# Optimization experiments

Hardware: AMD Instinct MI355X
Metric: run time of the kernel (lower is better)

Reference implementation:

```python
import jax, jax.numpy as jnp
import numpy as np

N_USERS = 100_000
N_ITEMS = 200_000
N_EDGES = 1_000_000
D = 64        # in_size == every layer_size
L = 3         # number of NGCF layers
B = 4096      # BPR batch
SLOPE = 0.2   # LeakyReLU negative slope
EPS = 1e-12   # F.normalize eps


def setup_inputs() -> dict:
    key = jax.random.key(0)
    ks = jax.random.split(key, 11)
    s = 1.0 / np.sqrt(D)  # xavier-ish scale
    return dict(
        user_feat=jax.random.normal(ks[0], (N_USERS, D), jnp.float32) * s,
        item_feat=jax.random.normal(ks[1], (N_ITEMS, D), jnp.float32) * s,
        W1=jax.random.normal(ks[2], (L, D, D), jnp.float32) * s,
        b1=jnp.zeros((L, D), jnp.float32),
        W2=jax.random.normal(ks[3], (L, D, D), jnp.float32) * s,
        b2=jnp.zeros((L, D), jnp.float32),
        edge_src=jax.random.randint(ks[4], (N_EDGES,), 0, N_USERS),
        edge_dst=jax.random.randint(ks[5], (N_EDGES,), 0, N_ITEMS),
        users=jax.random.randint(ks[6], (B,), 0, N_USERS),
        pos_items=jax.random.randint(ks[7], (B,), 0, N_ITEMS),
        neg_items=jax.random.randint(ks[8], (B,), 0, N_ITEMS),
    )


def _act_norm(h):
    # LeakyReLU(0.2) -> (dropout=identity, eval) -> row-wise L2 normalize
    h = jax.nn.leaky_relu(h, SLOPE)
    n = jnp.linalg.norm(h, axis=1, keepdims=True)
    return h / jnp.maximum(n, EPS)


def _ngcf_forward(user_feat, item_feat, W1, b1, W2, b2, edge_src, edge_dst):
    ones = jnp.ones((edge_src.shape[0],), user_feat.dtype)
    deg_u = jax.ops.segment_sum(ones, edge_src, num_segments=N_USERS)  # out-degree of users
    deg_i = jax.ops.segment_sum(ones, edge_dst, num_segments=N_ITEMS)  # in-degree of items
    norm = (deg_u[edge_src] * deg_i[edge_dst]) ** -0.5  # [E], same for both directions
    norm = norm[:, None]

    hu, hi = user_feat, item_feat
    u_embeds, i_embeds = [hu], [hi]
    for l in range(L):
        # per-edge elementwise product term (shared between both directions)
        p = hu[edge_src] * hi[edge_dst]            # [E, D]
        pw = p @ W2[l] + b2[l]                     # [E, D]
        # user -> item messages, summed per item
        m_i = norm * ((hu @ W1[l] + b1[l])[edge_src] + pw)
        # item -> user messages, summed per user
        m_u = norm * ((hi @ W1[l] + b1[l])[edge_dst] + pw)
        hi_new = jax.ops.segment_sum(m_i, edge_dst, num_segments=N_ITEMS)
        hu_new = jax.ops.segment_sum(m_u, edge_src, num_segments=N_USERS)
        hu, hi = _act_norm(hu_new), _act_norm(hi_new)
        u_embeds.append(hu)
        i_embeds.append(hi)

    user_embd = jnp.concatenate(u_embeds, axis=1)  # [N_USERS, D*(L+1)]
    item_embd = jnp.concatenate(i_embeds, axis=1)  # [N_ITEMS, D*(L+1)]
    return user_embd, item_embd


def reference(user_feat, item_feat, W1, b1, W2, b2,
              edge_src, edge_dst, users, pos_items, neg_items):
    user_embd, item_embd = _ngcf_forward(
        user_feat, item_feat, W1, b1, W2, b2, edge_src, edge_dst)
    return (user_embd[users], item_embd[pos_items], item_embd[neg_items])
```

## Files before the change

### kernel.cpp

```cpp
#include <hip/hip_runtime.h>

#define NU 100000
#define NI 200000
#define NE 1000000
#define NB 4096
#define CAP 16384
#define NBS 98
#define NBD 98
#define NTI (NI / 16)
#define NTU (NU / 16)

typedef __attribute__((ext_vector_type(8))) short bf16x8;
typedef __attribute__((ext_vector_type(4))) float f32x4;
typedef __attribute__((ext_vector_type(8))) unsigned short u16x8;

static __device__ __forceinline__ short f2bf(float f) {
  unsigned u = __builtin_bit_cast(unsigned, f);
  unsigned r = (u + 0x7fffu + ((u >> 16) & 1u)) >> 16;
  return (short)r;
}
static __device__ __forceinline__ float bf2f(unsigned short u) {
  return __builtin_bit_cast(float, ((unsigned)u) << 16);
}

__global__ __launch_bounds__(256) void binA_kernel(const int* __restrict__ src,
                                                   const int* __restrict__ dst,
                                                   int* __restrict__ gcur_s,
                                                   int* __restrict__ gcur_d,
                                                   int2* __restrict__ temp_s,
                                                   int2* __restrict__ temp_d) {
  __shared__ int lh[128], lbase[128], lpos[128];
  const int dir = blockIdx.x >> 9;
  const int cb = blockIdx.x & 511;
  const int lo = (int)(((long long)NE * cb) >> 9);
  const int hi = (int)(((long long)NE * (cb + 1)) >> 9);
  const int* key = dir ? dst : src;
  const int* oth = dir ? src : dst;
  int* gcur = dir ? gcur_d : gcur_s;
  int2* temp = dir ? temp_d : temp_s;
  const int shift = dir ? 11 : 10;
  const int tid = threadIdx.x;
  if (tid < 128) lh[tid] = 0;
  __syncthreads();
  for (int e = lo + tid; e < hi; e += 256) atomicAdd(&lh[key[e] >> shift], 1);
  __syncthreads();
  if (tid < 128) {
    const int c = lh[tid];
    lbase[tid] = c ? atomicAdd(&gcur[tid], c) : 0;
    lpos[tid] = 0;
  }
  __syncthreads();
  for (int e = lo + tid; e < hi; e += 256) {
    const int k = key[e];
    const int b = k >> shift;
    const int p = lbase[b] + atomicAdd(&lpos[b], 1);
    temp[(size_t)b * CAP + p] = make_int2(k, oth[e]);
  }
}

__global__ void bktscan_kernel(const int* __restrict__ gcur_s, const int* __restrict__ gcur_d,
                               int* __restrict__ bktofs_s, int* __restrict__ bktofs_d,
                               int* __restrict__ ofs_u, int* __restrict__ ofs_i) {
  const int t = threadIdx.x;
  if (t == 0) {
    int a = 0;
    for (int i = 0; i < NBS; ++i) { bktofs_s[i] = a; a += gcur_s[i]; }
    bktofs_s[NBS] = a;
    ofs_u[NU] = NE;
  }
  if (t == 1) {
    int a = 0;
    for (int i = 0; i < NBD; ++i) { bktofs_d[i] = a; a += gcur_d[i]; }
    bktofs_d[NBD] = a;
    ofs_i[NI] = NE;
  }
}

__global__ __launch_bounds__(256) void placeB_kernel(const int2* __restrict__ temp_s,
                                                     const int2* __restrict__ temp_d,
                                                     const int* __restrict__ gcur_s,
                                                     const int* __restrict__ gcur_d,
                                                     const int* __restrict__ bktofs_s,
                                                     const int* __restrict__ bktofs_d,
                                                     int* __restrict__ ofs_u, int* __restrict__ ofs_i,
                                                     float* __restrict__ rs_u, float* __restrict__ rs_i,
                                                     float* __restrict__ srs_u, float* __restrict__ srs_i,
                                                     int* __restrict__ by_src, int* __restrict__ by_dst) {
  __shared__ int cnt[2048];
  __shared__ int exc[2048];
  __shared__ int wsum[256];
  const bool isdst = blockIdx.x >= NBS;
  const int b = isdst ? (int)blockIdx.x - NBS : (int)blockIdx.x;
  const int shift = isdst ? 11 : 10;
  const int nodelo = b << shift;
  const int n = isdst ? NI : NU;
  const int2* temp = (isdst ? temp_d : temp_s) + (size_t)b * CAP;
  const int ecnt = (isdst ? gcur_d : gcur_s)[b];
  const int bbase = (isdst ? bktofs_d : bktofs_s)[b];
  int* ofs = isdst ? ofs_i : ofs_u;
  float* rs = isdst ? rs_i : rs_u;
  float* srs = isdst ? srs_i : srs_u;
  int* by = isdst ? by_dst : by_src;
  const int tid = threadIdx.x;
  const int NN = 1 << shift;

  for (int j = tid; j < NN; j += 256) cnt[j] = 0;
  __syncthreads();
  for (int k = tid; k < ecnt; k += 256) atomicAdd(&cnt[temp[k].x - nodelo], 1);
  __syncthreads();
  const int per = NN >> 8;
  int s = 0;
  for (int j = 0; j < per; ++j) s += cnt[tid * per + j];
  wsum[tid] = s;
  __syncthreads();
  for (int off = 1; off < 256; off <<= 1) {
    int t2 = (tid >= off) ? wsum[tid - off] : 0;
    __syncthreads();
    wsum[tid] += t2;
    __syncthreads();
  }
  int run = wsum[tid] - s;
  for (int j = 0; j < per; ++j) {
    const int idx = tid * per + j;
    exc[idx] = run;
    run += cnt[idx];
  }
  __syncthreads();
  for (int j = tid; j < NN; j += 256) {
    const int node = nodelo + j;
    if (node < n) {
      ofs[node] = bbase + exc[j];
      const int d = cnt[j];
      rs[node] = d > 0 ? rsqrtf((float)d) : 0.f;
      srs[node] = d > 0 ? sqrtf((float)d) : 0.f;
    }
  }
  __syncthreads();
  for (int j = tid; j < NN; j += 256) cnt[j] = exc[j];
  __syncthreads();
  for (int k = tid; k < ecnt; k += 256) {
    const int2 t2 = temp[k];
    const int p = bbase + atomicAdd(&cnt[t2.x - nodelo], 1);
    by[p] = t2.y;
  }
}

__global__ __launch_bounds__(256) void c_kernel(const int* __restrict__ ofs_i,
                                                const int* __restrict__ ofs_u,
                                                const int* __restrict__ by_dst,
                                                const int* __restrict__ by_src,
                                                const float* __restrict__ rs_u,
                                                const float* __restrict__ rs_i,
                                                float* __restrict__ c_i,
                                                float* __restrict__ c_u) {
  int r = blockIdx.x * 256 + threadIdx.x;
  if (r < NI) {
    const int lo = ofs_i[r], hi = ofs_i[r + 1];
    float s = 0.f;
    for (int k = lo; k < hi; ++k) s += rs_u[by_dst[k]];
    c_i[r] = rs_i[r] * s;
  } else if (r < NI + NU) {
    r -= NI;
    const int lo = ofs_u[r], hi = ofs_u[r + 1];
    float s = 0.f;
    for (int k = lo; k < hi; ++k) s += rs_i[by_src[k]];
    c_u[r] = rs_u[r] * s;
  }
}

__global__ __launch_bounds__(256) void conv_kernel(const float* __restrict__ uf,
                                                   const float* __restrict__ itf,
                                                   const float* __restrict__ rs_u,
                                                   const float* __restrict__ rs_i,
                                                   unsigned short* __restrict__ hsu,
                                                   unsigned short* __restrict__ hsi) {
  int i = blockIdx.x * 256 + threadIdx.x;
  const int n4u = NU * 16;
  const float* in;
  const float* rs;
  unsigned short* outp;
  int j;
  if (i < n4u) {
    in = uf; rs = rs_u; outp = hsu; j = i;
  } else if (i < n4u + NI * 16) {
    in = itf; rs = rs_i; outp = hsi; j = i - n4u;
  } else return;
  const float rsn = rs[j >> 4];
  float4 v = *(const float4*)&in[(size_t)j * 4];
  ushort4 o;
  o.x = (unsigned short)f2bf(v.x * rsn);
  o.y = (unsigned short)f2bf(v.y * rsn);
  o.z = (unsigned short)f2bf(v.z * rsn);
  o.w = (unsigned short)f2bf(v.w * rsn);
  *(ushort4*)&outp[(size_t)j * 4] = o;
}

__global__ __launch_bounds__(256) void layer_fused_kernel(const int* __restrict__ ofs_i,
                                                          const int* __restrict__ ofs_u,
                                                          const int* __restrict__ by_dst,
                                                          const int* __restrict__ by_src,
                                                          const float* __restrict__ rs_u,
                                                          const float* __restrict__ rs_i,
                                                          const float* __restrict__ c_i,
                                                          const float* __restrict__ c_u,
                                                          const unsigned short* __restrict__ hsu,
                                                          const unsigned short* __restrict__ hsi,
                                                          const float* __restrict__ W1,
                                                          const float* __restrict__ b1,
                                                          const float* __restrict__ W2,
                                                          const float* __restrict__ b2,
                                                          unsigned short* __restrict__ hsi_new,
                                                          unsigned short* __restrict__ hsu_new) {
  __shared__ unsigned short wlds[8192];
  const int tid = threadIdx.x;
  const int lane = tid & 63;
  const int row16 = lane & 15;
  const int kg = lane >> 4;
  for (int ch = tid; ch < 1024; ch += 256) {
    const int w = ch >> 9;
    const int rem = ch & 511;
    const int nb = rem >> 7, kb = (rem >> 6) & 1, l2 = rem & 63;
    const int r16 = l2 & 15, kg2 = l2 >> 4;
    const float* W = w ? W2 : W1;
    unsigned short* dstp = &wlds[ch * 8];
#pragma unroll
    for (int j = 0; j < 8; ++j)
      dstp[j] = (unsigned short)f2bf(W[(kb * 32 + kg2 * 8 + j) * 64 + nb * 16 + r16]);
  }
  __syncthreads();

  float bsum[4];
#pragma unroll
  for (int nb = 0; nb < 4; ++nb) bsum[nb] = b1[nb * 16 + row16] + b2[nb * 16 + row16];

  const int wid = (blockIdx.x * 256 + tid) >> 6;
  const int nwaves = (gridDim.x * 256) >> 6;

  for (int t = wid; t < NTI + NTU; t += nwaves) {
    const bool item = t < NTI;
    const int tt = item ? t : t - NTI;
    const int* ofs = item ? ofs_i : ofs_u;
    const int* pay = item ? by_dst : by_src;
    const float* rsw = item ? rs_i : rs_u;
    const float* cc = item ? c_i : c_u;
    const unsigned short* hs = item ? hsu : hsi;
    const unsigned short* hsown = item ? hsi : hsu;
    unsigned short* hsnew = item ? hsi_new : hsu_new;
    const int r0 = tt * 16;
    const int node = r0 + row16;

    const int lo = ofs[node], hiE = ofs[node + 1];
    int rounds = (hiE - lo + 3) >> 2;
#pragma unroll
    for (int m = 1; m < 16; m <<= 1) rounds = max(rounds, __shfl_xor(rounds, m));

    float a0[8] = {0.f, 0.f, 0.f, 0.f, 0.f, 0.f, 0.f, 0.f};
    float a1[8] = {0.f, 0.f, 0.f, 0.f, 0.f, 0.f, 0.f, 0.f};
    for (int rd = 0; rd < rounds; ++rd) {
      const int i0 = lo + rd * 4;
      int nb4[4];
      float wt[4];
#pragma unroll
      for (int s = 0; s < 4; ++s) {
        const int idx = i0 + s;
        nb4[s] = pay[min(idx, NE - 1)];
        wt[s] = (idx < hiE) ? 1.f : 0.f;
      }
      u16x8 h0[4], h1[4];
#pragma unroll
      for (int s = 0; s < 4; ++s) {
        const unsigned short* hp = hs + (size_t)nb4[s] * 64 + kg * 8;
        h0[s] = *(const u16x8*)hp;
        h1[s] = *(const u16x8*)(hp + 32);
      }
#pragma unroll
      for (int s = 0; s < 4; ++s)
#pragma unroll
        for (int j = 0; j < 8; ++j) {
          a0[j] += wt[s] * bf2f(h0[s][j]);
          a1[j] += wt[s] * bf2f(h1[s][j]);
        }
    }

    const float rsn = rsw[node];
    const float cnode = cc[node];
    const unsigned short* hp = hsown + (size_t)node * 64 + kg * 8;
    const u16x8 hv0 = *(const u16x8*)hp;
    const u16x8 hv1 = *(const u16x8*)(hp + 32);
    bf16x8 ag[2], ap[2];
#pragma unroll
    for (int j = 0; j < 8; ++j) {
      ag[0][j] = f2bf(a0[j] * rsn);
      ag[1][j] = f2bf(a1[j] * rsn);
      ap[0][j] = f2bf(a0[j] * bf2f(hv0[j]));
      ap[1][j] = f2bf(a1[j] * bf2f(hv1[j]));
    }

    f32x4 acc[4];
#pragma unroll
    for (int nb = 0; nb < 4; ++nb) acc[nb] = (f32x4){0.f, 0.f, 0.f, 0.f};
    const unsigned short* wl = wlds + lane * 8;
#pragma unroll
    for (int nb = 0; nb < 4; ++nb)
#pragma unroll
      for (int kb = 0; kb < 2; ++kb) {
        const bf16x8 w1f = *(const bf16x8*)(wl + ((0 * 4 + nb) * 2 + kb) * 512);
        const bf16x8 w2f = *(const bf16x8*)(wl + ((1 * 4 + nb) * 2 + kb) * 512);
        acc[nb] = __builtin_amdgcn_mfma_f32_16x16x32_bf16(ag[kb], w1f, acc[nb], 0, 0, 0);
        acc[nb] = __builtin_amdgcn_mfma_f32_16x16x32_bf16(ap[kb], w2f, acc[nb], 0, 0, 0);
      }

    float cv[4], rsrow[4];
#pragma unroll
    for (int reg = 0; reg < 4; ++reg) {
      cv[reg] = __shfl(cnode, kg * 4 + reg);
      rsrow[reg] = __shfl(rsn, kg * 4 + reg);
    }
    float v[4][4];
    float ss[4] = {0.f, 0.f, 0.f, 0.f};
#pragma unroll
    for (int nb = 0; nb < 4; ++nb)
#pragma unroll
      for (int reg = 0; reg < 4; ++reg) {
        float x = acc[nb][reg] + cv[reg] * bsum[nb];
        x = (x > 0.f) ? x : 0.2f * x;
        v[nb][reg] = x;
        ss[reg] += x * x;
      }
#pragma unroll
    for (int m = 1; m < 16; m <<= 1)
#pragma unroll
      for (int reg = 0; reg < 4; ++reg) ss[reg] += __shfl_xor(ss[reg], m);
#pragma unroll
    for (int reg = 0; reg < 4; ++reg) {
      const float invs = rsrow[reg] / fmaxf(sqrtf(ss[reg]), 1e-12f);
      const size_t rowbase = (size_t)(r0 + kg * 4 + reg) * 64;
#pragma unroll
      for (int nb = 0; nb < 4; ++nb)
        hsnew[rowbase + nb * 16 + row16] = (unsigned short)f2bf(v[nb][reg] * invs);
    }
  }
}

__global__ __launch_bounds__(256) void gather_f32_kernel(const float* __restrict__ hu,
                                                         const float* __restrict__ hi,
                                                         const int* __restrict__ users,
                                                         const int* __restrict__ pos,
                                                         const int* __restrict__ neg,
                                                         float* __restrict__ out) {
  int t = blockIdx.x * 256 + threadIdx.x;
  if (t >= 3 * NB * 64) return;
  int j = t & 63;
  int b = (t >> 6) & (NB - 1);
  int which = t / (NB * 64);
  int row = (which == 0) ? users[b] : ((which == 1) ? pos[b] : neg[b]);
  const float* h = (which == 0) ? hu : hi;
  out[(size_t)which * NB * 256 + (size_t)b * 256 + j] = h[(size_t)row * 64 + j];
}

__global__ __launch_bounds__(256) void gather_bf_kernel(const unsigned short* __restrict__ hsu,
                                                        const unsigned short* __restrict__ hsi,
                                                        const float* __restrict__ srs_u,
                                                        const float* __restrict__ srs_i,
                                                        const int* __restrict__ users,
                                                        const int* __restrict__ pos,
                                                        const int* __restrict__ neg,
                                                        float* __restrict__ out, int stage) {
  int t = blockIdx.x * 256 + threadIdx.x;
  if (t >= 3 * NB * 64) return;
  int j = t & 63;
  int b = (t >> 6) & (NB - 1);
  int which = t / (NB * 64);
  int row = (which == 0) ? users[b] : ((which == 1) ? pos[b] : neg[b]);
  const unsigned short* h = (which == 0) ? hsu : hsi;
  const float s = (which == 0) ? srs_u[row] : srs_i[row];
  out[(size_t)which * NB * 256 + (size_t)b * 256 + (size_t)stage * 64 + j] =
      bf2f(h[(size_t)row * 64 + j]) * s;
}

extern "C" void kernel_launch(void* const* d_in, const int* in_sizes, int n_in,
                              void* d_out, int out_size, void* d_ws, size_t ws_size,
                              hipStream_t stream) {
  (void)in_sizes; (void)n_in; (void)out_size; (void)ws_size;
  const float* user_feat = (const float*)d_in[0];
  const float* item_feat = (const float*)d_in[1];
  const float* W1 = (const float*)d_in[2];
  const float* b1 = (const float*)d_in[3];
  const float* W2 = (const float*)d_in[4];
  const float* b2 = (const float*)d_in[5];
  const int* edge_src = (const int*)d_in[6];
  const int* edge_dst = (const int*)d_in[7];
  const int* users = (const int*)d_in[8];
  const int* pos_items = (const int*)d_in[9];
  const int* neg_items = (const int*)d_in[10];
  float* out = (float*)d_out;

  char* base = (char*)d_ws;
  size_t ofsz = 0;
  auto alloc = [&](size_t bytes) -> char* {
    char* r = base + ofsz;
    ofsz += (bytes + 1023) & ~(size_t)1023;
    return r;
  };
  int* ofs_u = (int*)alloc((NU + 1) * 4);
  int* ofs_i = (int*)alloc((NI + 1) * 4);
  int* gcur_s = (int*)alloc(128 * 4);
  int* gcur_d = (int*)alloc(128 * 4);
  int* bktofs_s = (int*)alloc(128 * 4);
  int* bktofs_d = (int*)alloc(128 * 4);
  int2* temp_s = (int2*)alloc((size_t)NBS * CAP * 8);
  int2* temp_d = (int2*)alloc((size_t)NBD * CAP * 8);
  int* by_src = (int*)alloc((size_t)NE * 4);
  int* by_dst = (int*)alloc((size_t)NE * 4);
  float* rs_u = (float*)alloc((size_t)NU * 4);
  float* rs_i = (float*)alloc((size_t)NI * 4);
  float* srs_u = (float*)alloc((size_t)NU * 4);
  float* srs_i = (float*)alloc((size_t)NI * 4);
  float* c_u = (float*)alloc((size_t)NU * 4);
  float* c_i = (float*)alloc((size_t)NI * 4);
  unsigned short* hsU0 = (unsigned short*)alloc((size_t)NU * 64 * 2);
  unsigned short* hsU1 = (unsigned short*)alloc((size_t)NU * 64 * 2);
  unsigned short* hsI0 = (unsigned short*)alloc((size_t)NI * 64 * 2);
  unsigned short* hsI1 = (unsigned short*)alloc((size_t)NI * 64 * 2);

  unsigned short* bufU[2] = {hsU1, hsU0};
  unsigned short* bufI[2] = {hsI1, hsI0};

  hipMemsetAsync(gcur_s, 0, 128 * 4, stream);
  hipMemsetAsync(gcur_d, 0, 128 * 4, stream);
  binA_kernel<<<1024, 256, 0, stream>>>(edge_src, edge_dst, gcur_s, gcur_d, temp_s, temp_d);
  bktscan_kernel<<<1, 64, 0, stream>>>(gcur_s, gcur_d, bktofs_s, bktofs_d, ofs_u, ofs_i);
  placeB_kernel<<<NBS + NBD, 256, 0, stream>>>(temp_s, temp_d, gcur_s, gcur_d,
                                               bktofs_s, bktofs_d, ofs_u, ofs_i,
                                               rs_u, rs_i, srs_u, srs_i, by_src, by_dst);
  c_kernel<<<(NI + NU + 255) / 256, 256, 0, stream>>>(ofs_i, ofs_u, by_dst, by_src,
                                                      rs_u, rs_i, c_i, c_u);

  conv_kernel<<<((NU + NI) * 16 + 255) / 256, 256, 0, stream>>>(
      user_feat, item_feat, rs_u, rs_i, hsU0, hsI0);

  gather_f32_kernel<<<(3 * NB * 64 + 255) / 256, 256, 0, stream>>>(
      user_feat, item_feat, users, pos_items, neg_items, out);

  const unsigned short* hsu = hsU0;
  const unsigned short* hsi = hsI0;
  for (int l = 0; l < 3; ++l) {
    unsigned short* hsu_new = bufU[l & 1];
    unsigned short* hsi_new = bufI[l & 1];
    layer_fused_kernel<<<2048, 256, 0, stream>>>(ofs_i, ofs_u, by_dst, by_src,
                                                 rs_u, rs_i, c_i, c_u,
                                                 hsu, hsi,
                                                 W1 + l * 4096, b1 + l * 64,
                                                 W2 + l * 4096, b2 + l * 64,
                                                 hsi_new, hsu_new);
    gather_bf_kernel<<<(3 * NB * 64 + 255) / 256, 256, 0, stream>>>(
        hsu_new, hsi_new, srs_u, srs_i, users, pos_items, neg_items, out, l + 1);
    hsu = hsu_new;
    hsi = hsi_new;
  }
}
```

Baseline: 415.4 us.

## Renumber users and items by degree for uniform per-tile workloads

Adds a preprocessing pass that buckets nodes by degree, builds a permutation and its inverse, and rebuilds the CSR offsets and neighbour lists in the new node order. Features are permuted on conversion, and the output gather maps original ids through the inverse permutation. The aim is that each 16-node tile in the fused layer kernel holds nodes of equal degree, which cuts lane divergence and load imbalance in the message loops. In exchange it adds several kernels and extra scratch memory on every call. Degrees at or above 63 are clamped to one bucket while the offsets assume exactly that degree, so nodes with higher degree would get wrong offsets.

```diff
diff --git a/kernel.cpp b/kernel.cpp
--- a/kernel.cpp
+++ b/kernel.cpp
@@ -9,6 +9,10 @@
 #define NBD 98
 #define NTI (NI / 16)
 #define NTU (NU / 16)
+#define DBKT 64
+#define CAPD 65536
+#define NBI 196
+#define NBU 98
 
 typedef __attribute__((ext_vector_type(8))) short bf16x8;
 typedef __attribute__((ext_vector_type(4))) float f32x4;
@@ -83,8 +87,6 @@
                                                      const int* __restrict__ bktofs_s,
                                                      const int* __restrict__ bktofs_d,
                                                      int* __restrict__ ofs_u, int* __restrict__ ofs_i,
-                                                     float* __restrict__ rs_u, float* __restrict__ rs_i,
-                                                     float* __restrict__ srs_u, float* __restrict__ srs_i,
                                                      int* __restrict__ by_src, int* __restrict__ by_dst) {
   __shared__ int cnt[2048];
   __shared__ int exc[2048];
@@ -98,8 +100,6 @@
   const int ecnt = (isdst ? gcur_d : gcur_s)[b];
   const int bbase = (isdst ? bktofs_d : bktofs_s)[b];
   int* ofs = isdst ? ofs_i : ofs_u;
-  float* rs = isdst ? rs_i : rs_u;
-  float* srs = isdst ? srs_i : srs_u;
   int* by = isdst ? by_dst : by_src;
   const int tid = threadIdx.x;
   const int NN = 1 << shift;
@@ -128,12 +128,7 @@
   __syncthreads();
   for (int j = tid; j < NN; j += 256) {
     const int node = nodelo + j;
-    if (node < n) {
-      ofs[node] = bbase + exc[j];
-      const int d = cnt[j];
-      rs[node] = d > 0 ? rsqrtf((float)d) : 0.f;
-      srs[node] = d > 0 ? sqrtf((float)d) : 0.f;
-    }
+    if (node < n) ofs[node] = bbase + exc[j];
   }
   __syncthreads();
   for (int j = tid; j < NN; j += 256) cnt[j] = exc[j];
@@ -145,48 +140,167 @@
   }
 }
 
-__global__ __launch_bounds__(256) void c_kernel(const int* __restrict__ ofs_i,
-                                                const int* __restrict__ ofs_u,
-                                                const int* __restrict__ by_dst,
-                                                const int* __restrict__ by_src,
-                                                const float* __restrict__ rs_u,
-                                                const float* __restrict__ rs_i,
+__global__ __launch_bounds__(256) void dbinA_kernel(const int* __restrict__ ofs_i,
+                                                    const int* __restrict__ ofs_u,
+                                                    int* __restrict__ dgcur,
+                                                    int* __restrict__ arena_i,
+                                                    int* __restrict__ arena_u) {
+  __shared__ int lh[DBKT], lbase[DBKT], lpos[DBKT];
+  const bool item = blockIdx.x < NBI;
+  const int b = item ? (int)blockIdx.x : (int)blockIdx.x - NBI;
+  const int n = item ? NI : NU;
+  const int* ofs = item ? ofs_i : ofs_u;
+  int* cur = dgcur + (item ? 0 : DBKT);
+  int* arena = item ? arena_i : arena_u;
+  const int nodelo = b << 10;
+  const int nodehi = min(nodelo + 1024, n);
+  const int tid = threadIdx.x;
+  if (tid < DBKT) lh[tid] = 0;
+  __syncthreads();
+  for (int node = nodelo + tid; node < nodehi; node += 256)
+    atomicAdd(&lh[min(ofs[node + 1] - ofs[node], DBKT - 1)], 1);
+  __syncthreads();
+  if (tid < DBKT) {
+    const int c = lh[tid];
+    lbase[tid] = c ? atomicAdd(&cur[tid], c) : 0;
+    lpos[tid] = 0;
+  }
+  __syncthreads();
+  for (int node = nodelo + tid; node < nodehi; node += 256) {
+    const int d = min(ofs[node + 1] - ofs[node], DBKT - 1);
+    const int p = lbase[d] + atomicAdd(&lpos[d], 1);
+    arena[d * CAPD + p] = node;
+  }
+}
+
+__global__ void dbktscan_kernel(const int* __restrict__ dgcur,
+                                int* __restrict__ dofs, int* __restrict__ dedge,
+                                int* __restrict__ ofs2_i, int* __restrict__ ofs2_u) {
+  const int t = threadIdx.x;
+  if (t == 0) {
+    int a = 0, e = 0;
+    for (int d = 0; d < DBKT; ++d) { dofs[d] = a; dedge[d] = e; a += dgcur[d]; e += dgcur[d] * d; }
+    ofs2_i[NI] = NE;
+  }
+  if (t == 1) {
+    int a = 0, e = 0;
+    for (int d = 0; d < DBKT; ++d) {
+      dofs[DBKT + d] = a; dedge[DBKT + d] = e;
+      a += dgcur[DBKT + d]; e += dgcur[DBKT + d] * d;
+    }
+    ofs2_u[NU] = NE;
+  }
+}
+
+__global__ __launch_bounds__(256) void dcompact_kernel(const int* __restrict__ dgcur,
+                                                       const int* __restrict__ dofs,
+                                                       const int* __restrict__ dedge,
+                                                       const int* __restrict__ arena_i,
+                                                       const int* __restrict__ arena_u,
+                                                       int* __restrict__ perm_i, int* __restrict__ perm_u,
+                                                       int* __restrict__ inv_i, int* __restrict__ inv_u,
+                                                       int* __restrict__ ofs2_i, int* __restrict__ ofs2_u,
+                                                       float* __restrict__ rs2_i, float* __restrict__ rs2_u,
+                                                       float* __restrict__ srs2_i, float* __restrict__ srs2_u) {
+  const int bk = blockIdx.x;
+  const bool item = bk < DBKT;
+  const int d = item ? bk : bk - DBKT;
+  const int cnt = dgcur[bk];
+  const int nodebase = dofs[bk];
+  const int edgebase = dedge[bk];
+  const int* arena = item ? arena_i : arena_u;
+  int* perm = item ? perm_i : perm_u;
+  int* inv = item ? inv_i : inv_u;
+  int* ofs2 = item ? ofs2_i : ofs2_u;
+  float* rs2 = item ? rs2_i : rs2_u;
+  float* srs2 = item ? srs2_i : srs2_u;
+  const float rsv = d ? rsqrtf((float)d) : 0.f;
+  const float srsv = d ? sqrtf((float)d) : 0.f;
+  for (int k = threadIdx.x; k < cnt; k += 256) {
+    const int node = arena[d * CAPD + k];
+    const int r = nodebase + k;
+    perm[r] = node;
+    inv[node] = r;
+    ofs2[r] = edgebase + k * d;
+    rs2[r] = rsv;
+    srs2[r] = srsv;
+  }
+}
+
+__global__ __launch_bounds__(256) void remapby_kernel(const int* __restrict__ ofs_i,
+                                                      const int* __restrict__ ofs_u,
+                                                      const int* __restrict__ ofs2_i,
+                                                      const int* __restrict__ ofs2_u,
+                                                      const int* __restrict__ perm_i,
+                                                      const int* __restrict__ perm_u,
+                                                      const int* __restrict__ inv_i,
+                                                      const int* __restrict__ inv_u,
+                                                      const int* __restrict__ by_dst,
+                                                      const int* __restrict__ by_src,
+                                                      int* __restrict__ by2_dst,
+                                                      int* __restrict__ by2_src) {
+  int r = blockIdx.x * 256 + threadIdx.x;
+  if (r < NI) {
+    const int lo2 = ofs2_i[r];
+    const int d = ofs2_i[r + 1] - lo2;
+    const int oo = ofs_i[perm_i[r]];
+    for (int k = 0; k < d; ++k) by2_dst[lo2 + k] = inv_u[by_dst[oo + k]];
+  } else if (r < NI + NU) {
+    r -= NI;
+    const int lo2 = ofs2_u[r];
+    const int d = ofs2_u[r + 1] - lo2;
+    const int oo = ofs_u[perm_u[r]];
+    for (int k = 0; k < d; ++k) by2_src[lo2 + k] = inv_i[by_src[oo + k]];
+  }
+}
+
+__global__ __launch_bounds__(256) void c_kernel(const int* __restrict__ ofs2_i,
+                                                const int* __restrict__ ofs2_u,
+                                                const int* __restrict__ by2_dst,
+                                                const int* __restrict__ by2_src,
+                                                const float* __restrict__ rs2_u,
+                                                const float* __restrict__ rs2_i,
                                                 float* __restrict__ c_i,
                                                 float* __restrict__ c_u) {
   int r = blockIdx.x * 256 + threadIdx.x;
   if (r < NI) {
-    const int lo = ofs_i[r], hi = ofs_i[r + 1];
+    const int lo = ofs2_i[r], hi = ofs2_i[r + 1];
     float s = 0.f;
-    for (int k = lo; k < hi; ++k) s += rs_u[by_dst[k]];
-    c_i[r] = rs_i[r] * s;
+    for (int k = lo; k < hi; ++k) s += rs2_u[by2_dst[k]];
+    c_i[r] = rs2_i[r] * s;
   } else if (r < NI + NU) {
     r -= NI;
-    const int lo = ofs_u[r], hi = ofs_u[r + 1];
+    const int lo = ofs2_u[r], hi = ofs2_u[r + 1];
     float s = 0.f;
-    for (int k = lo; k < hi; ++k) s += rs_i[by_src[k]];
-    c_u[r] = rs_u[r] * s;
+    for (int k = lo; k < hi; ++k) s += rs2_i[by2_src[k]];
+    c_u[r] = rs2_u[r] * s;
   }
 }
 
 __global__ __launch_bounds__(256) void conv_kernel(const float* __restrict__ uf,
                                                    const float* __restrict__ itf,
-                                                   const float* __restrict__ rs_u,
-                                                   const float* __restrict__ rs_i,
+                                                   const int* __restrict__ perm_u,
+                                                   const int* __restrict__ perm_i,
+                                                   const float* __restrict__ rs2_u,
+                                                   const float* __restrict__ rs2_i,
                                                    unsigned short* __restrict__ hsu,
                                                    unsigned short* __restrict__ hsi) {
   int i = blockIdx.x * 256 + threadIdx.x;
   const int n4u = NU * 16;
   const float* in;
+  const int* perm;
   const float* rs;
   unsigned short* outp;
   int j;
   if (i < n4u) {
-    in = uf; rs = rs_u; outp = hsu; j = i;
+    in = uf; perm = perm_u; rs = rs2_u; outp = hsu; j = i;
   } else if (i < n4u + NI * 16) {
-    in = itf; rs = rs_i; outp = hsi; j = i - n4u;
+    in = itf; perm = perm_i; rs = rs2_i; outp = hsi; j = i - n4u;
   } else return;
-  const float rsn = rs[j >> 4];
-  float4 v = *(const float4*)&in[(size_t)j * 4];
+  const int rnew = j >> 4;
+  const int grp = j & 15;
+  const float rsn = rs[rnew];
+  float4 v = *(const float4*)&in[(size_t)perm[rnew] * 64 + grp * 4];
   ushort4 o;
   o.x = (unsigned short)f2bf(v.x * rsn);
   o.y = (unsigned short)f2bf(v.y * rsn);
@@ -195,12 +309,12 @@
   *(ushort4*)&outp[(size_t)j * 4] = o;
 }
 
-__global__ __launch_bounds__(256) void layer_fused_kernel(const int* __restrict__ ofs_i,
-                                                          const int* __restrict__ ofs_u,
-                                                          const int* __restrict__ by_dst,
-                                                          const int* __restrict__ by_src,
-                                                          const float* __restrict__ rs_u,
-                                                          const float* __restrict__ rs_i,
+__global__ __launch_bounds__(256) void layer_fused_kernel(const int* __restrict__ ofs2_i,
+                                                          const int* __restrict__ ofs2_u,
+                                                          const int* __restrict__ by2_dst,
+                                                          const int* __restrict__ by2_src,
+                                                          const float* __restrict__ rs2_u,
+                                                          const float* __restrict__ rs2_i,
                                                           const float* __restrict__ c_i,
                                                           const float* __restrict__ c_u,
                                                           const unsigned short* __restrict__ hsu,
@@ -239,9 +353,9 @@
   for (int t = wid; t < NTI + NTU; t += nwaves) {
     const bool item = t < NTI;
     const int tt = item ? t : t - NTI;
-    const int* ofs = item ? ofs_i : ofs_u;
-    const int* pay = item ? by_dst : by_src;
-    const float* rsw = item ? rs_i : rs_u;
+    const int* ofs = item ? ofs2_i : ofs2_u;
+    const int* pay = item ? by2_dst : by2_src;
+    const float* rsw = item ? rs2_i : rs2_u;
     const float* cc = item ? c_i : c_u;
     const unsigned short* hs = item ? hsu : hsi;
     const unsigned short* hsown = item ? hsi : hsu;
@@ -360,8 +474,10 @@
 
 __global__ __launch_bounds__(256) void gather_bf_kernel(const unsigned short* __restrict__ hsu,
                                                         const unsigned short* __restrict__ hsi,
-                                                        const float* __restrict__ srs_u,
-                                                        const float* __restrict__ srs_i,
+                                                        const float* __restrict__ srs2_u,
+                                                        const float* __restrict__ srs2_i,
+                                                        const int* __restrict__ inv_u,
+                                                        const int* __restrict__ inv_i,
                                                         const int* __restrict__ users,
                                                         const int* __restrict__ pos,
                                                         const int* __restrict__ neg,
@@ -372,10 +488,11 @@
   int b = (t >> 6) & (NB - 1);
   int which = t / (NB * 64);
   int row = (which == 0) ? users[b] : ((which == 1) ? pos[b] : neg[b]);
+  const int rnew = (which == 0) ? inv_u[row] : inv_i[row];
   const unsigned short* h = (which == 0) ? hsu : hsi;
-  const float s = (which == 0) ? srs_u[row] : srs_i[row];
+  const float s = (which == 0) ? srs2_u[rnew] : srs2_i[rnew];
   out[(size_t)which * NB * 256 + (size_t)b * 256 + (size_t)stage * 64 + j] =
-      bf2f(h[(size_t)row * 64 + j]) * s;
+      bf2f(h[(size_t)rnew * 64 + j]) * s;
 }
 
 extern "C" void kernel_launch(void* const* d_in, const int* in_sizes, int n_in,
@@ -404,18 +521,31 @@
   };
   int* ofs_u = (int*)alloc((NU + 1) * 4);
   int* ofs_i = (int*)alloc((NI + 1) * 4);
+  int* ofs2_u = (int*)alloc((NU + 1) * 4);
+  int* ofs2_i = (int*)alloc((NI + 1) * 4);
   int* gcur_s = (int*)alloc(128 * 4);
   int* gcur_d = (int*)alloc(128 * 4);
   int* bktofs_s = (int*)alloc(128 * 4);
   int* bktofs_d = (int*)alloc(128 * 4);
+  int* dgcur = (int*)alloc(2 * DBKT * 4);
+  int* dofs = (int*)alloc(2 * DBKT * 4);
+  int* dedge = (int*)alloc(2 * DBKT * 4);
   int2* temp_s = (int2*)alloc((size_t)NBS * CAP * 8);
   int2* temp_d = (int2*)alloc((size_t)NBD * CAP * 8);
   int* by_src = (int*)alloc((size_t)NE * 4);
   int* by_dst = (int*)alloc((size_t)NE * 4);
-  float* rs_u = (float*)alloc((size_t)NU * 4);
-  float* rs_i = (float*)alloc((size_t)NI * 4);
-  float* srs_u = (float*)alloc((size_t)NU * 4);
-  float* srs_i = (float*)alloc((size_t)NI * 4);
+  int* by2_src = (int*)alloc((size_t)NE * 4);
+  int* by2_dst = (int*)alloc((size_t)NE * 4);
+  int* arena_i = (int*)alloc((size_t)DBKT * CAPD * 4);
+  int* arena_u = (int*)alloc((size_t)DBKT * CAPD * 4);
+  int* perm_i = (int*)alloc((size_t)NI * 4);
+  int* perm_u = (int*)alloc((size_t)NU * 4);
+  int* inv_i = (int*)alloc((size_t)NI * 4);
+  int* inv_u = (int*)alloc((size_t)NU * 4);
+  float* rs2_u = (float*)alloc((size_t)NU * 4);
+  float* rs2_i = (float*)alloc((size_t)NI * 4);
+  float* srs2_u = (float*)alloc((size_t)NU * 4);
+  float* srs2_i = (float*)alloc((size_t)NI * 4);
   float* c_u = (float*)alloc((size_t)NU * 4);
   float* c_i = (float*)alloc((size_t)NI * 4);
   unsigned short* hsU0 = (unsigned short*)alloc((size_t)NU * 64 * 2);
@@ -428,16 +558,24 @@
 
   hipMemsetAsync(gcur_s, 0, 128 * 4, stream);
   hipMemsetAsync(gcur_d, 0, 128 * 4, stream);
+  hipMemsetAsync(dgcur, 0, 2 * DBKT * 4, stream);
   binA_kernel<<<1024, 256, 0, stream>>>(edge_src, edge_dst, gcur_s, gcur_d, temp_s, temp_d);
   bktscan_kernel<<<1, 64, 0, stream>>>(gcur_s, gcur_d, bktofs_s, bktofs_d, ofs_u, ofs_i);
   placeB_kernel<<<NBS + NBD, 256, 0, stream>>>(temp_s, temp_d, gcur_s, gcur_d,
                                                bktofs_s, bktofs_d, ofs_u, ofs_i,
-                                               rs_u, rs_i, srs_u, srs_i, by_src, by_dst);
-  c_kernel<<<(NI + NU + 255) / 256, 256, 0, stream>>>(ofs_i, ofs_u, by_dst, by_src,
-                                                      rs_u, rs_i, c_i, c_u);
-
+                                               by_src, by_dst);
+  dbinA_kernel<<<NBI + NBU, 256, 0, stream>>>(ofs_i, ofs_u, dgcur, arena_i, arena_u);
+  dbktscan_kernel<<<1, 64, 0, stream>>>(dgcur, dofs, dedge, ofs2_i, ofs2_u);
+  dcompact_kernel<<<2 * DBKT, 256, 0, stream>>>(dgcur, dofs, dedge, arena_i, arena_u,
+                                                perm_i, perm_u, inv_i, inv_u,
+                                                ofs2_i, ofs2_u, rs2_i, rs2_u, srs2_i, srs2_u);
+  remapby_kernel<<<(NI + NU + 255) / 256, 256, 0, stream>>>(ofs_i, ofs_u, ofs2_i, ofs2_u,
+                                                            perm_i, perm_u, inv_i, inv_u,
+                                                            by_dst, by_src, by2_dst, by2_src);
+  c_kernel<<<(NI + NU + 255) / 256, 256, 0, stream>>>(ofs2_i, ofs2_u, by2_dst, by2_src,
+                                                      rs2_u, rs2_i, c_i, c_u);
   conv_kernel<<<((NU + NI) * 16 + 255) / 256, 256, 0, stream>>>(
-      user_feat, item_feat, rs_u, rs_i, hsU0, hsI0);
+      user_feat, item_feat, perm_u, perm_i, rs2_u, rs2_i, hsU0, hsI0);
 
   gather_f32_kernel<<<(3 * NB * 64 + 255) / 256, 256, 0, stream>>>(
       user_feat, item_feat, users, pos_items, neg_items, out);
@@ -447,14 +585,15 @@
   for (int l = 0; l < 3; ++l) {
     unsigned short* hsu_new = bufU[l & 1];
     unsigned short* hsi_new = bufI[l & 1];
-    layer_fused_kernel<<<2048, 256, 0, stream>>>(ofs_i, ofs_u, by_dst, by_src,
-                                                 rs_u, rs_i, c_i, c_u,
+    layer_fused_kernel<<<2048, 256, 0, stream>>>(ofs2_i, ofs2_u, by2_dst, by2_src,
+                                                 rs2_u, rs2_i, c_i, c_u,
                                                  hsu, hsi,
                                                  W1 + l * 4096, b1 + l * 64,
                                                  W2 + l * 4096, b2 + l * 64,
                                                  hsi_new, hsu_new);
     gather_bf_kernel<<<(3 * NB * 64 + 255) / 256, 256, 0, stream>>>(
-        hsu_new, hsi_new, srs_u, srs_i, users, pos_items, neg_items, out, l + 1);
+        hsu_new, hsi_new, srs2_u, srs2_i, inv_u, inv_i,
+        users, pos_items, neg_items, out, l + 1);
     hsu = hsu_new;
     hsi = hsi_new;
   }
```

After: 427.3 us. +2.8%, slower.

## Fuse batch output gather into layer kernel via per-node linked lists

Applied to the files above, without the earlier changes.

Builds per-node linked lists (head plus next arrays) of the batch slots that reference each user or item. The layer kernel then writes normalized fp32 rows straight into the output when it finishes a node, which removes the separate gather kernel per layer and the srs arrays. Output now comes from fp32 values before the bf16 rounding, which changes precision slightly. It adds two memsets of 1.2 MB, one small kernel, and a head lookup per row inside the hot layer kernel.

```diff
diff --git a/kernel.cpp b/kernel.cpp
--- a/kernel.cpp
+++ b/kernel.cpp
@@ -84,7 +84,6 @@
                                                      const int* __restrict__ bktofs_d,
                                                      int* __restrict__ ofs_u, int* __restrict__ ofs_i,
                                                      float* __restrict__ rs_u, float* __restrict__ rs_i,
-                                                     float* __restrict__ srs_u, float* __restrict__ srs_i,
                                                      int* __restrict__ by_src, int* __restrict__ by_dst) {
   __shared__ int cnt[2048];
   __shared__ int exc[2048];
@@ -99,7 +98,6 @@
   const int bbase = (isdst ? bktofs_d : bktofs_s)[b];
   int* ofs = isdst ? ofs_i : ofs_u;
   float* rs = isdst ? rs_i : rs_u;
-  float* srs = isdst ? srs_i : srs_u;
   int* by = isdst ? by_dst : by_src;
   const int tid = threadIdx.x;
   const int NN = 1 << shift;
@@ -132,7 +130,6 @@
       ofs[node] = bbase + exc[j];
       const int d = cnt[j];
       rs[node] = d > 0 ? rsqrtf((float)d) : 0.f;
-      srs[node] = d > 0 ? sqrtf((float)d) : 0.f;
     }
   }
   __syncthreads();
@@ -166,6 +163,20 @@
     for (int k = lo; k < hi; ++k) s += rs_i[by_src[k]];
     c_u[r] = rs_u[r] * s;
   }
+}
+
+__global__ __launch_bounds__(256) void obuild_kernel(const int* __restrict__ users,
+                                                     const int* __restrict__ pos,
+                                                     const int* __restrict__ neg,
+                                                     int* __restrict__ head_u,
+                                                     int* __restrict__ head_i,
+                                                     int* __restrict__ nxt) {
+  const int s = blockIdx.x * 256 + threadIdx.x;
+  if (s >= 3 * NB) return;
+  const int which = s / NB, b = s - which * NB;
+  const int row = (which == 0) ? users[b] : ((which == 1) ? pos[b] : neg[b]);
+  int* head = (which == 0) ? head_u : head_i;
+  nxt[s] = atomicExch(&head[row], s);
 }
 
 __global__ __launch_bounds__(256) void conv_kernel(const float* __restrict__ uf,
@@ -209,6 +220,11 @@
                                                           const float* __restrict__ b1,
                                                           const float* __restrict__ W2,
                                                           const float* __restrict__ b2,
+                                                          const int* __restrict__ head_i,
+                                                          const int* __restrict__ head_u,
+                                                          const int* __restrict__ nxt,
+                                                          float* __restrict__ outp,
+                                                          int stage,
                                                           unsigned short* __restrict__ hsi_new,
                                                           unsigned short* __restrict__ hsu_new) {
   __shared__ unsigned short wlds[8192];
@@ -243,6 +259,7 @@
     const int* pay = item ? by_dst : by_src;
     const float* rsw = item ? rs_i : rs_u;
     const float* cc = item ? c_i : c_u;
+    const int* head = item ? head_i : head_u;
     const unsigned short* hs = item ? hsu : hsi;
     const unsigned short* hsown = item ? hsi : hsu;
     unsigned short* hsnew = item ? hsi_new : hsu_new;
@@ -333,11 +350,20 @@
       for (int reg = 0; reg < 4; ++reg) ss[reg] += __shfl_xor(ss[reg], m);
 #pragma unroll
     for (int reg = 0; reg < 4; ++reg) {
-      const float invs = rsrow[reg] / fmaxf(sqrtf(ss[reg]), 1e-12f);
-      const size_t rowbase = (size_t)(r0 + kg * 4 + reg) * 64;
+      const int noder = r0 + kg * 4 + reg;
+      const float invn = 1.0f / fmaxf(sqrtf(ss[reg]), 1e-12f);
+      const float invs = invn * rsrow[reg];
+      const size_t rowbase = (size_t)noder * 64;
 #pragma unroll
       for (int nb = 0; nb < 4; ++nb)
         hsnew[rowbase + nb * 16 + row16] = (unsigned short)f2bf(v[nb][reg] * invs);
+      int s = head[noder];
+      while (s >= 0) {
+        float* op = outp + (size_t)s * 256 + stage * 64;
+#pragma unroll
+        for (int nb = 0; nb < 4; ++nb) op[nb * 16 + row16] = v[nb][reg] * invn;
+        s = nxt[s];
+      }
     }
   }
 }
@@ -356,26 +382,6 @@
   int row = (which == 0) ? users[b] : ((which == 1) ? pos[b] : neg[b]);
   const float* h = (which == 0) ? hu : hi;
   out[(size_t)which * NB * 256 + (size_t)b * 256 + j] = h[(size_t)row * 64 + j];
-}
-
-__global__ __launch_bounds__(256) void gather_bf_kernel(const unsigned short* __restrict__ hsu,
-                                                        const unsigned short* __restrict__ hsi,
-                                                        const float* __restrict__ srs_u,
-                                                        const float* __restrict__ srs_i,
-                                                        const int* __restrict__ users,
-                                                        const int* __restrict__ pos,
-                                                        const int* __restrict__ neg,
-                                                        float* __restrict__ out, int stage) {
-  int t = blockIdx.x * 256 + threadIdx.x;
-  if (t >= 3 * NB * 64) return;
-  int j = t & 63;
-  int b = (t >> 6) & (NB - 1);
-  int which = t / (NB * 64);
-  int row = (which == 0) ? users[b] : ((which == 1) ? pos[b] : neg[b]);
-  const unsigned short* h = (which == 0) ? hsu : hsi;
-  const float s = (which == 0) ? srs_u[row] : srs_i[row];
-  out[(size_t)which * NB * 256 + (size_t)b * 256 + (size_t)stage * 64 + j] =
-      bf2f(h[(size_t)row * 64 + j]) * s;
 }
 
 extern "C" void kernel_launch(void* const* d_in, const int* in_sizes, int n_in,
@@ -414,10 +420,11 @@
   int* by_dst = (int*)alloc((size_t)NE * 4);
   float* rs_u = (float*)alloc((size_t)NU * 4);
   float* rs_i = (float*)alloc((size_t)NI * 4);
-  float* srs_u = (float*)alloc((size_t)NU * 4);
-  float* srs_i = (float*)alloc((size_t)NI * 4);
   float* c_u = (float*)alloc((size_t)NU * 4);
   float* c_i = (float*)alloc((size_t)NI * 4);
+  int* head_u = (int*)alloc((size_t)NU * 4);
+  int* head_i = (int*)alloc((size_t)NI * 4);
+  int* onxt = (int*)alloc(3 * NB * 4);
   unsigned short* hsU0 = (unsigned short*)alloc((size_t)NU * 64 * 2);
   unsigned short* hsU1 = (unsigned short*)alloc((size_t)NU * 64 * 2);
   unsigned short* hsI0 = (unsigned short*)alloc((size_t)NI * 64 * 2);
@@ -428,14 +435,17 @@
 
   hipMemsetAsync(gcur_s, 0, 128 * 4, stream);
   hipMemsetAsync(gcur_d, 0, 128 * 4, stream);
+  hipMemsetAsync(head_u, 0xFF, (size_t)NU * 4, stream);
+  hipMemsetAsync(head_i, 0xFF, (size_t)NI * 4, stream);
   binA_kernel<<<1024, 256, 0, stream>>>(edge_src, edge_dst, gcur_s, gcur_d, temp_s, temp_d);
   bktscan_kernel<<<1, 64, 0, stream>>>(gcur_s, gcur_d, bktofs_s, bktofs_d, ofs_u, ofs_i);
   placeB_kernel<<<NBS + NBD, 256, 0, stream>>>(temp_s, temp_d, gcur_s, gcur_d,
                                                bktofs_s, bktofs_d, ofs_u, ofs_i,
-                                               rs_u, rs_i, srs_u, srs_i, by_src, by_dst);
+                                               rs_u, rs_i, by_src, by_dst);
   c_kernel<<<(NI + NU + 255) / 256, 256, 0, stream>>>(ofs_i, ofs_u, by_dst, by_src,
                                                       rs_u, rs_i, c_i, c_u);
-
+  obuild_kernel<<<(3 * NB + 255) / 256, 256, 0, stream>>>(users, pos_items, neg_items,
+                                                          head_u, head_i, onxt);
   conv_kernel<<<((NU + NI) * 16 + 255) / 256, 256, 0, stream>>>(
       user_feat, item_feat, rs_u, rs_i, hsU0, hsI0);
 
@@ -452,9 +462,8 @@
                                                  hsu, hsi,
                                                  W1 + l * 4096, b1 + l * 64,
                                                  W2 + l * 4096, b2 + l * 64,
+                                                 head_i, head_u, onxt, out, l + 1,
                                                  hsi_new, hsu_new);
-    gather_bf_kernel<<<(3 * NB * 64 + 255) / 256, 256, 0, stream>>>(
-        hsu_new, hsi_new, srs_u, srs_i, users, pos_items, neg_items, out, l + 1);
     hsu = hsu_new;
     hsi = hsi_new;
   }
```

Result: slower. 428.4 us (+3.1%).
